# Kernel tuning notes

Hardware: AMD Instinct MI355X
Metric: run time of the kernel (lower is better)

## Reference

```python
import jax, jax.numpy as jnp
import numpy as np

B, S, D = 8, 512, 1024
E, F, K = 8, 4096, 2


def setup_inputs() -> dict:
    key = jax.random.key(0)
    ks = jax.random.split(key, 8)
    scale = 1.0 / np.sqrt(D)
    return {
        "x": jax.random.normal(ks[0], (B, S, D), jnp.float32),
        "y": jax.random.randint(ks[1], (B,), 0, D),
        "W": jax.random.normal(ks[2], (D, D), jnp.float32) * scale,
        "b": jnp.zeros((D,), jnp.float32),
        "Wg": jax.random.normal(ks[3], (D, E), jnp.float32) * scale,
        "w1": jax.random.normal(ks[4], (E, D, F), jnp.float32) * scale,
        "b1": jnp.zeros((E, F), jnp.float32),
        "w2": jax.random.normal(ks[5], (E, F, D), jnp.float32) * (1.0 / np.sqrt(F)),
        "b2": jnp.zeros((E, D), jnp.float32),
    }


def reference(x, y, W, b, Wg, w1, b1, w2, b2):
    # linear projection (torch Linear convention: x @ W.T + b)
    lin = jnp.einsum("bsd,ed->bse", x, W) + b                      # [B,S,D]

    # --- MoE: top-2 softmax gate, renormalized over the top-k ---
    gate_logits = jnp.einsum("bsd,de->bse", lin, Wg)               # [B,S,E]
    probs = jax.nn.softmax(gate_logits, axis=-1)
    top_p, top_i = jax.lax.top_k(probs, K)                          # [B,S,K]
    top_p = top_p / jnp.sum(top_p, axis=-1, keepdims=True)
    # combine weights per expert: scatter top-k probs back to [B,S,E]
    gate = jnp.sum(jax.nn.one_hot(top_i, E, dtype=lin.dtype) * top_p[..., None], axis=-2)  # [B,S,E]

    # expert FFNs evaluated densely, combined by (sparse) gate weights
    h = jax.nn.relu(jnp.einsum("bsd,edf->ebsf", lin, w1) + b1[:, None, None, :])  # [E,B,S,F]
    expert_out = jnp.einsum("ebsf,efd->ebsd", h, w2) + b2[:, None, None, :]        # [E,B,S,D]
    moe_out = jnp.einsum("bse,ebsd->bsd", gate, expert_out)                        # [B,S,D]

    # residual, mean pool over sequence, cross-entropy
    sent_emb = jnp.mean(x + moe_out, axis=1)                       # [B,D] used as logits
    logp = jax.nn.log_softmax(sent_emb, axis=-1)
    loss = -jnp.mean(logp[jnp.arange(B), y])
    return loss
```

## Files before the change

kernel.cpp:

```cpp
#include <hip/hip_runtime.h>

#define TOK 4096
#define DD  1024
#define NE  8
#define FF  4096
#define NB  8
#define SS  512
#define HROWS 8320

typedef unsigned short ushort_t;
typedef __attribute__((ext_vector_type(8))) short bshort8;
typedef __attribute__((ext_vector_type(4))) float floatx4;

__device__ __forceinline__ ushort_t f2bf(float f) {
  unsigned int u = __float_as_uint(f);
  u += 0x7fffu + ((u >> 16) & 1u);
  return (ushort_t)(u >> 16);
}
__device__ __forceinline__ float bf2f(ushort_t h) {
  return __uint_as_float(((unsigned int)h) << 16);
}

__device__ __forceinline__ void gl_lds16(const ushort_t* g, ushort_t* l) {
  __builtin_amdgcn_global_load_lds(
      (const __attribute__((address_space(1))) unsigned int*)g,
      (__attribute__((address_space(3))) unsigned int*)l, 16, 0, 0);
}

__global__ __launch_bounds__(256) void k_cast(
    const float* __restrict__ in, ushort_t* __restrict__ out, int n4) {
  int i = blockIdx.x * 256 + threadIdx.x;
  if (i < n4) {
    float4 v = ((const float4*)in)[i];
    ushort4 o;
    o.x = f2bf(v.x); o.y = f2bf(v.y); o.z = f2bf(v.z); o.w = f2bf(v.w);
    ((ushort4*)out)[i] = o;
  }
}

__global__ __launch_bounds__(256) void k_transpose_cast(
    const float* __restrict__ in, size_t in_estride, int in_rstride,
    ushort_t* __restrict__ out, size_t out_estride, int out_rstride) {
  __shared__ ushort_t t[64][70];
  const float* ib = in + blockIdx.z * in_estride;
  ushort_t* ob = out + blockIdx.z * out_estride;
  const int r0 = blockIdx.y * 64, c0 = blockIdx.x * 64;
  const int tid = threadIdx.x;
  const int lr = tid >> 4, lc4 = (tid & 15) * 4;
#pragma unroll
  for (int it = 0; it < 4; ++it) {
    int r = lr + it * 16;
    float4 v = *(const float4*)&ib[(size_t)(r0 + r) * in_rstride + c0 + lc4];
    t[r][lc4 + 0] = f2bf(v.x);
    t[r][lc4 + 1] = f2bf(v.y);
    t[r][lc4 + 2] = f2bf(v.z);
    t[r][lc4 + 3] = f2bf(v.w);
  }
  __syncthreads();
  const int oc = tid >> 5, od2 = (tid & 31) * 2;
#pragma unroll
  for (int it = 0; it < 8; ++it) {
    int cc = oc + it * 8;
    ushort2 w;
    w.x = t[od2 + 0][cc];
    w.y = t[od2 + 1][cc];
    *(ushort2*)&ob[(size_t)(c0 + cc) * out_rstride + r0 + od2] = w;
  }
}

template <int MODE>
__global__ __launch_bounds__(256) void k_mfma(
    const ushort_t* __restrict__ A, const ushort_t* __restrict__ Bm,
    const float* __restrict__ bias, ushort_t* __restrict__ Obf,
    float* __restrict__ Of, const int* __restrict__ cnt,
    const int* __restrict__ offs, const int* __restrict__ btok, int f0,
    int accum, int kext, int ast, int ost, size_t bstride) {
  const int e = (MODE == 0) ? 0 : blockIdx.z;
  int c = TOK, off = 0;
  if (MODE != 0) {
    c = cnt[e];
    off = offs[e];
    if ((int)blockIdx.y * 128 >= c) return;
  }
  const int m0 = blockIdx.y * 128;
  const int n0 = blockIdx.x * 128;
  const ushort_t* Bp = (MODE == 0) ? Bm : Bm + (size_t)e * bstride;

  __shared__ ushort_t Als[128 * 32];
  __shared__ ushort_t Bls[128 * 32];
  __shared__ int ts[128];

  const int tid = threadIdx.x;
  if (tid < 128) {
    int p = m0 + tid;
    int r;
    if (MODE == 0) r = p;
    else if (MODE == 1) r = btok[e * TOK + min(p, c - 1)];
    else r = off + p;
    ts[tid] = r;
  }

  const int lane = tid & 63;
  const int w = tid >> 6;
  const int wm = (w & 1) * 64, wn = (w >> 1) * 64;
  const int lm = lane & 15, lq = lane >> 4;
  const int sr = lane >> 2;
  const int sg = lane & 3;

  floatx4 zero = {0.f, 0.f, 0.f, 0.f};
  floatx4 acc[4][4];
#pragma unroll
  for (int i = 0; i < 4; ++i)
#pragma unroll
    for (int j = 0; j < 4; ++j) acc[i][j] = zero;

  for (int k0 = 0; k0 < kext; k0 += 32) {
    __syncthreads();
#pragma unroll
    for (int i = 0; i < 2; ++i) {
      int r = w * 32 + i * 16 + sr;
      int q = (sg - (r >> 1)) & 3;
      const ushort_t* src = A + (size_t)ts[r] * ast + k0 + q * 8;
      ushort_t* dst = Als + r * 32 + sg * 8;
      gl_lds16(src, dst);
    }
#pragma unroll
    for (int i = 0; i < 2; ++i) {
      int r = w * 32 + i * 16 + sr;
      int q = (sg - (r >> 1)) & 3;
      const ushort_t* src = Bp + (size_t)(n0 + r) * kext + k0 + q * 8;
      ushort_t* dst = Bls + r * 32 + sg * 8;
      gl_lds16(src, dst);
    }
    __syncthreads();

    bshort8 af[4], bfr[4];
#pragma unroll
    for (int i = 0; i < 4; ++i) {
      int r = wm + i * 16 + lm;
      af[i] = *(const bshort8*)&Als[r * 32 + (((lq + (r >> 1)) & 3) * 8)];
    }
#pragma unroll
    for (int j = 0; j < 4; ++j) {
      int r = wn + j * 16 + lm;
      bfr[j] = *(const bshort8*)&Bls[r * 32 + (((lq + (r >> 1)) & 3) * 8)];
    }
#pragma unroll
    for (int i = 0; i < 4; ++i)
#pragma unroll
      for (int j = 0; j < 4; ++j)
        acc[i][j] = __builtin_amdgcn_mfma_f32_16x16x32_bf16(af[i], bfr[j],
                                                            acc[i][j], 0, 0, 0);
  }

#pragma unroll
  for (int i = 0; i < 4; ++i) {
#pragma unroll
    for (int j = 0; j < 4; ++j) {
      int n = wn + j * 16 + lm;
#pragma unroll
      for (int rr = 0; rr < 4; ++rr) {
        int m = wm + i * 16 + lq * 4 + rr;
        float v = acc[i][j][rr];
        if (MODE == 0) {
          int gn = n0 + n;
          v += bias[gn];
          Obf[(size_t)(m0 + m) * DD + gn] = f2bf(v);
        } else if (MODE == 1) {
          int p = m0 + m;
          if (p < c) {
            int gn = n0 + n;
            v += bias[(size_t)e * FF + f0 + gn];
            v = fmaxf(v, 0.f);
            Obf[(size_t)(off + p) * ost + gn] = f2bf(v);
          }
        } else {
          int p = m0 + m;
          if (p < c) {
            int gn = n0 + n;
            if (!accum) v += bias[(size_t)e * DD + gn];
            float* dp = &Of[(size_t)(off + p) * DD + gn];
            if (accum) *dp += v; else *dp = v;
          }
        }
      }
    }
  }
}

__global__ __launch_bounds__(256) void k_logits(
    const ushort_t* __restrict__ lin_bf, const float* __restrict__ Wg,
    int* __restrict__ topi, float* __restrict__ wts) {
  const int wv = threadIdx.x >> 6, lane = threadIdx.x & 63;
  const int t = blockIdx.x * 4 + wv;
  float acc[NE] = {};
  const ushort_t* lr = lin_bf + (size_t)t * DD;
#pragma unroll 4
  for (int d0 = 0; d0 < DD; d0 += 64) {
    float v = bf2f(lr[d0 + lane]);
    const float* wgr = Wg + (size_t)(d0 + lane) * NE;
    float4 g0 = *(const float4*)(wgr);
    float4 g1 = *(const float4*)(wgr + 4);
    acc[0] += v * g0.x; acc[1] += v * g0.y; acc[2] += v * g0.z; acc[3] += v * g0.w;
    acc[4] += v * g1.x; acc[5] += v * g1.y; acc[6] += v * g1.z; acc[7] += v * g1.w;
  }
#pragma unroll
  for (int off = 32; off > 0; off >>= 1) {
#pragma unroll
    for (int e = 0; e < NE; ++e) acc[e] += __shfl_xor(acc[e], off);
  }
  if (lane == 0) {
    int i1 = 0;
#pragma unroll
    for (int e = 1; e < NE; ++e)
      if (acc[e] > acc[i1]) i1 = e;
    int i2 = (i1 == 0) ? 1 : 0;
#pragma unroll
    for (int e = 0; e < NE; ++e)
      if (e != i1 && acc[e] > acc[i2]) i2 = e;
    float r = __expf(acc[i2] - acc[i1]);
    topi[t] = i1 | (i2 << 4);
    wts[2 * t + 0] = 1.0f / (1.0f + r);
    wts[2 * t + 1] = r / (1.0f + r);
  }
}

#define RT 512
__global__ __launch_bounds__(RT) void k_route(
    const int* __restrict__ topi, int* __restrict__ cnt, int* __restrict__ offs,
    int* __restrict__ btok, int* __restrict__ eslot) {
  __shared__ int sc[NE][RT + 1];
  __shared__ int tot[NE];
  const int tid = threadIdx.x;
  int lc[NE] = {};
  int my[8];
#pragma unroll
  for (int i = 0; i < 8; ++i) {
    int t = tid * 8 + i;
    int p = topi[t];
    my[i] = p;
    lc[p & 15]++;
    lc[(p >> 4) & 15]++;
  }
#pragma unroll
  for (int e = 0; e < NE; ++e) sc[e][tid] = lc[e];
  __syncthreads();
  if (tid < NE) {
    int s = 0;
    for (int i = 0; i < RT; ++i) { int v = sc[tid][i]; sc[tid][i] = s; s += v; }
    tot[tid] = s;
  }
  __syncthreads();
  if (tid == 0) {
    int s = 0;
    for (int e = 0; e < NE; ++e) { offs[e] = s; cnt[e] = tot[e]; s += tot[e]; }
  }
  __syncthreads();
  int run[NE];
#pragma unroll
  for (int e = 0; e < NE; ++e) run[e] = sc[e][tid];
#pragma unroll
  for (int i = 0; i < 8; ++i) {
    int t = tid * 8 + i, p = my[i];
    int e1 = p & 15, e2 = (p >> 4) & 15;
    int s1 = run[e1]++;
    btok[e1 * TOK + s1] = t;
    eslot[2 * t + 0] = e1 * TOK + s1;
    int s2 = run[e2]++;
    btok[e2 * TOK + s2] = t;
    eslot[2 * t + 1] = e2 * TOK + s2;
  }
}

__global__ __launch_bounds__(256) void k_pool(
    const float* __restrict__ x, const float* __restrict__ ob,
    const int* __restrict__ offs, const int* __restrict__ eslot,
    const float* __restrict__ wts, float* __restrict__ sent) {
  const int b = blockIdx.y;
  const int d = blockIdx.x * 256 + threadIdx.x;
  const int sc = blockIdx.z;
  float a = 0.f;
  for (int s = sc * 64; s < sc * 64 + 64; ++s) {
    int t = b * SS + s;
    int e0 = eslot[2 * t], e1 = eslot[2 * t + 1];
    int g0 = offs[e0 >> 12] + (e0 & (TOK - 1));
    int g1 = offs[e1 >> 12] + (e1 & (TOK - 1));
    a += x[(size_t)t * DD + d] + wts[2 * t] * ob[(size_t)g0 * DD + d] +
         wts[2 * t + 1] * ob[(size_t)g1 * DD + d];
  }
  atomicAdd(&sent[b * DD + d], a * (1.0f / SS));
}

__global__ __launch_bounds__(1024) void k_loss(
    const float* __restrict__ sent, const int* __restrict__ y,
    float* __restrict__ out) {
  __shared__ float red[16];
  const int tid = threadIdx.x;
  const int lane = tid & 63, wv = tid >> 6;
  float loss = 0.f;
  for (int b = 0; b < NB; ++b) {
    float v = sent[b * DD + tid];
    float m = v;
#pragma unroll
    for (int off = 32; off > 0; off >>= 1) m = fmaxf(m, __shfl_xor(m, off));
    if (lane == 0) red[wv] = m;
    __syncthreads();
    float m2 = red[0];
#pragma unroll
    for (int w = 1; w < 16; ++w) m2 = fmaxf(m2, red[w]);
    __syncthreads();
    float ex = __expf(v - m2);
#pragma unroll
    for (int off = 32; off > 0; off >>= 1) ex += __shfl_xor(ex, off);
    if (lane == 0) red[wv] = ex;
    __syncthreads();
    if (tid == 0) {
      float se = 0.f;
      for (int w = 0; w < 16; ++w) se += red[w];
      loss += m2 + logf(se) - sent[b * DD + y[b]];
    }
    __syncthreads();
  }
  if (tid == 0) out[0] = loss / NB;
}

extern "C" void kernel_launch(void* const* d_in, const int* in_sizes, int n_in,
                              void* d_out, int out_size, void* d_ws,
                              size_t ws_size, hipStream_t stream) {
  const float* x  = (const float*)d_in[0];
  const int*   y  = (const int*)d_in[1];
  const float* W  = (const float*)d_in[2];
  const float* bb = (const float*)d_in[3];
  const float* Wg = (const float*)d_in[4];
  const float* w1 = (const float*)d_in[5];
  const float* b1 = (const float*)d_in[6];
  const float* w2 = (const float*)d_in[7];
  const float* b2 = (const float*)d_in[8];
  float* out = (float*)d_out;

  auto need = [](size_t FCr) -> size_t {
    size_t o = 0;
    auto al = [&](size_t b) { o = (o + b + 255) & ~255ull; };
    al((size_t)TOK * DD * 2);
    al((size_t)TOK * DD * 2);
    al((size_t)DD * DD * 2);
    al((size_t)HROWS * FCr * 2);
    al((size_t)NE * FCr * DD * 2);
    al((size_t)NE * DD * FCr * 2);
    al((size_t)HROWS * DD * 4);
    al((size_t)NE * TOK * 4);
    al(64); al(64);
    al((size_t)TOK * 4);
    al((size_t)2 * TOK * 4);
    al((size_t)2 * TOK * 4);
    al((size_t)NB * DD * 4);
    return o;
  };
  const int nchunks = (ws_size >= need(FF)) ? 1 : 4;
  const int FCr = FF / nchunks;

  char* base = (char*)d_ws;
  size_t o = 0;
  auto al = [&](size_t b) -> char* {
    char* p = base + o;
    o = (o + b + 255) & ~255ull;
    return p;
  };
  ushort_t* lin_bf = (ushort_t*)al((size_t)TOK * DD * 2);
  ushort_t* x_bf   = (ushort_t*)al((size_t)TOK * DD * 2);
  ushort_t* W_bf   = (ushort_t*)al((size_t)DD * DD * 2);
  ushort_t* h_bf   = (ushort_t*)al((size_t)HROWS * FCr * 2);
  ushort_t* w1t    = (ushort_t*)al((size_t)NE * FCr * DD * 2);
  ushort_t* w2t    = (ushort_t*)al((size_t)NE * DD * FCr * 2);
  float*    ob     = (float*)al((size_t)HROWS * DD * 4);
  int*      btok   = (int*)al((size_t)NE * TOK * 4);
  int*      cnt    = (int*)al(64);
  int*      offs   = (int*)al(64);
  int*      topi   = (int*)al((size_t)TOK * 4);
  int*      eslot  = (int*)al((size_t)2 * TOK * 4);
  float*    wts    = (float*)al((size_t)2 * TOK * 4);
  float*    sent   = (float*)al((size_t)NB * DD * 4);

  hipMemsetAsync(sent, 0, NB * DD * sizeof(float), stream);

  k_cast<<<TOK * DD / 4 / 256, 256, 0, stream>>>(x, x_bf, TOK * DD / 4);
  k_cast<<<DD * DD / 4 / 256, 256, 0, stream>>>(W, W_bf, DD * DD / 4);

  k_mfma<0><<<dim3(DD / 128, TOK / 128), 256, 0, stream>>>(
      x_bf, W_bf, bb, lin_bf, nullptr, nullptr, nullptr, nullptr, 0, 0,
      DD, DD, DD, 0);

  k_logits<<<TOK / 4, 256, 0, stream>>>(lin_bf, Wg, topi, wts);
  k_route<<<1, RT, 0, stream>>>(topi, cnt, offs, btok, eslot);

  for (int ci = 0; ci < nchunks; ++ci) {
    int f0 = ci * FCr;
    k_transpose_cast<<<dim3(FCr / 64, DD / 64, NE), 256, 0, stream>>>(
        w1 + f0, (size_t)DD * FF, FF, w1t, (size_t)FCr * DD, DD);
    k_mfma<1><<<dim3(FCr / 128, TOK / 128, NE), 256, 0, stream>>>(
        lin_bf, w1t, b1, h_bf, nullptr, cnt, offs, btok, f0, 0,
        DD, DD, FCr, (size_t)FCr * DD);
    k_transpose_cast<<<dim3(DD / 64, FCr / 64, NE), 256, 0, stream>>>(
        w2 + (size_t)f0 * DD, (size_t)FF * DD, DD, w2t, (size_t)DD * FCr, FCr);
    k_mfma<2><<<dim3(DD / 128, TOK / 128, NE), 256, 0, stream>>>(
        h_bf, w2t, b2, nullptr, ob, cnt, offs, btok, f0, ci > 0 ? 1 : 0,
        FCr, FCr, DD, (size_t)DD * FCr);
  }

  k_pool<<<dim3(DD / 256, NB, 8), 256, 0, stream>>>(x, ob, offs, eslot, wts,
                                                    sent);
  k_loss<<<1, 1024, 0, stream>>>(sent, y, out);
}
```

Baseline: 687.1 us.

## Double-buffer LDS tiles to overlap global loads with MFMA compute

Splits the A and B shared-memory tiles into two buffers and prefetches the next K-slice with global_load_lds while MFMAs run on the current slice, so each iteration needs one barrier instead of two. Per-thread source and destination addresses are hoisted out of the loop. This aims to hide global-memory latency in the grouped GEMM kernel. In exchange it doubles LDS use, which may lower occupancy, and correctness depends on __syncthreads waiting for the outstanding async LDS loads.

```diff
diff --git a/kernel.cpp b/kernel.cpp
--- a/kernel.cpp
+++ b/kernel.cpp
@@ -86,8 +86,8 @@
   const int n0 = blockIdx.x * 128;
   const ushort_t* Bp = (MODE == 0) ? Bm : Bm + (size_t)e * bstride;
 
-  __shared__ ushort_t Als[128 * 32];
-  __shared__ ushort_t Bls[128 * 32];
+  __shared__ ushort_t Als[2][128 * 32];
+  __shared__ ushort_t Bls[2][128 * 32];
   __shared__ int ts[128];
 
   const int tid = threadIdx.x;
@@ -99,6 +99,7 @@
     else r = off + p;
     ts[tid] = r;
   }
+  __syncthreads();
 
   const int lane = tid & 63;
   const int w = tid >> 6;
@@ -107,6 +108,24 @@
   const int sr = lane >> 2;
   const int sg = lane & 3;
 
+  const int r0 = w * 32 + sr;
+  const int r1 = r0 + 16;
+  const int q = (sg - (r0 >> 1)) & 3;
+  const int d0 = r0 * 32 + sg * 8;
+  const int d1 = r1 * 32 + sg * 8;
+  const ushort_t* sA0 = A + (size_t)ts[r0] * ast + q * 8;
+  const ushort_t* sA1 = A + (size_t)ts[r1] * ast + q * 8;
+  const ushort_t* sB0 = Bp + (size_t)(n0 + r0) * kext + q * 8;
+  const ushort_t* sB1 = Bp + (size_t)(n0 + r1) * kext + q * 8;
+
+#define STG(bi, kk)                       \
+  do {                                    \
+    gl_lds16(sA0 + (kk), &Als[bi][d0]);   \
+    gl_lds16(sA1 + (kk), &Als[bi][d1]);   \
+    gl_lds16(sB0 + (kk), &Bls[bi][d0]);   \
+    gl_lds16(sB1 + (kk), &Bls[bi][d1]);   \
+  } while (0)
+
   floatx4 zero = {0.f, 0.f, 0.f, 0.f};
   floatx4 acc[4][4];
 #pragma unroll
@@ -114,36 +133,25 @@
 #pragma unroll
     for (int j = 0; j < 4; ++j) acc[i][j] = zero;
 
+  STG(0, 0);
+  __syncthreads();
+
+  int cur = 0;
   for (int k0 = 0; k0 < kext; k0 += 32) {
-    __syncthreads();
-#pragma unroll
-    for (int i = 0; i < 2; ++i) {
-      int r = w * 32 + i * 16 + sr;
-      int q = (sg - (r >> 1)) & 3;
-      const ushort_t* src = A + (size_t)ts[r] * ast + k0 + q * 8;
-      ushort_t* dst = Als + r * 32 + sg * 8;
-      gl_lds16(src, dst);
-    }
-#pragma unroll
-    for (int i = 0; i < 2; ++i) {
-      int r = w * 32 + i * 16 + sr;
-      int q = (sg - (r >> 1)) & 3;
-      const ushort_t* src = Bp + (size_t)(n0 + r) * kext + k0 + q * 8;
-      ushort_t* dst = Bls + r * 32 + sg * 8;
-      gl_lds16(src, dst);
-    }
-    __syncthreads();
-
+    if (k0 + 32 < kext) STG(cur ^ 1, k0 + 32);
+
+    const ushort_t* Ab = Als[cur];
+    const ushort_t* Bb = Bls[cur];
     bshort8 af[4], bfr[4];
 #pragma unroll
     for (int i = 0; i < 4; ++i) {
       int r = wm + i * 16 + lm;
-      af[i] = *(const bshort8*)&Als[r * 32 + (((lq + (r >> 1)) & 3) * 8)];
+      af[i] = *(const bshort8*)&Ab[r * 32 + (((lq + (r >> 1)) & 3) * 8)];
     }
 #pragma unroll
     for (int j = 0; j < 4; ++j) {
       int r = wn + j * 16 + lm;
-      bfr[j] = *(const bshort8*)&Bls[r * 32 + (((lq + (r >> 1)) & 3) * 8)];
+      bfr[j] = *(const bshort8*)&Bb[r * 32 + (((lq + (r >> 1)) & 3) * 8)];
     }
 #pragma unroll
     for (int i = 0; i < 4; ++i)
@@ -151,7 +159,11 @@
       for (int j = 0; j < 4; ++j)
         acc[i][j] = __builtin_amdgcn_mfma_f32_16x16x32_bf16(af[i], bfr[j],
                                                             acc[i][j], 0, 0, 0);
-  }
+
+    __syncthreads();
+    cur ^= 1;
+  }
+#undef STG
 
 #pragma unroll
   for (int i = 0; i < 4; ++i) {
```

Result: faster. 647.6 us (-5.8%).
